# Performance work log

Measured on AMD Instinct MI355X. Metric: run time of the kernel, lower is better.

Reference implementation:

```python
import jax, jax.numpy as jnp
import numpy as np

N = 60000      # num_nodes
R = 70         # num_relations
B = 30         # num_bases
E = 1920000    # num_edges (avg degree 32)
STD = 0.1


def setup_inputs() -> dict:
    key = jax.random.key(0)
    ks = jax.random.split(key, 14)
    p = lambda k, shape: (jax.random.normal(k, shape, jnp.float32) * STD)
    inp = {}
    inp['edge_index'] = jax.random.randint(ks[0], (2, E), 0, N, dtype=jnp.int32)
    inp['edge_type'] = jax.random.randint(ks[1], (E,), 0, R, dtype=jnp.int32)
    # layer 1: in=N (identity features), out=32
    inp['att1'] = p(ks[2], (R, B))
    inp['basis1'] = p(ks[3], (B, N, 32))
    inp['root1'] = p(ks[4], (N, 32))
    inp['bias1'] = jnp.zeros((32,), jnp.float32)
    # layer 2: in=32, out=8
    inp['att2'] = p(ks[5], (R, B))
    inp['basis2'] = p(ks[6], (B, 32, 8))
    inp['root2'] = p(ks[7], (32, 8))
    inp['bias2'] = jnp.zeros((8,), jnp.float32)
    # layer 3: in=8, out=1
    inp['att3'] = p(ks[8], (R, B))
    inp['basis3'] = p(ks[9], (B, 8, 1))
    inp['root3'] = p(ks[10], (8, 1))
    inp['bias3'] = jnp.zeros((1,), jnp.float32)
    return inp


def _scatter_mean(msg, dst, num_nodes):
    s = jax.ops.segment_sum(msg, dst, num_segments=num_nodes)          # [N, O]
    cnt = jax.ops.segment_sum(jnp.ones((msg.shape[0], 1), msg.dtype), dst,
                              num_segments=num_nodes)                   # [N, 1]
    return s / jnp.maximum(cnt, 1.0)


def _rgcn(x, edge_index, edge_type, att, basis, root, bias, num_nodes):
    # basis decomposition: weight[r] = sum_b att[r,b] * basis[b]
    weight = jnp.einsum('rb,bio->rio', att, basis)  # [R, in, out]
    src, dst = edge_index[0], edge_index[1]
    if x is None:
        # identity input features -> message is a row of the relation weight
        msg = weight[edge_type, src]                # [E, out]
        self_term = root                            # x @ root with x = I
    else:
        # compute per-relation transforms once, then gather per edge
        h = jnp.einsum('ni,rio->rno', x, weight)    # [R, N, out]
        msg = h[edge_type, src]                     # [E, out]
        self_term = x @ root                        # [N, out]
    aggr = _scatter_mean(msg, dst, num_nodes)       # mean aggregation (old PyG RGCNConv)
    return aggr + self_term + bias


def reference(edge_index, edge_type, att1, basis1, root1, bias1,
              att2, basis2, root2, bias2, att3, basis3, root3, bias3):
    x = jax.nn.relu(_rgcn(None, edge_index, edge_type, att1, basis1, root1, bias1, N))
    x = jax.nn.relu(_rgcn(x, edge_index, edge_type, att2, basis2, root2, bias2, N))
    x = _rgcn(x, edge_index, edge_type, att3, basis3, root3, bias3, N)
    return x  # [N, 1]
```

## Files before the change

### kernel.cpp

```cpp
#include <hip/hip_runtime.h>
#include <hip/hip_bf16.h>
#include <hip/hip_fp16.h>

#define NNODES 60000
#define NREL   70
#define NB     30
#define NEDGE  1920000
#define NBLK   235
#define W2P    328

typedef _Float16 half2v __attribute__((ext_vector_type(2)));

static __device__ __forceinline__ float fdot2f(unsigned a, unsigned b, float c) {
    return __builtin_amdgcn_fdot2(__builtin_bit_cast(half2v, a),
                                  __builtin_bit_cast(half2v, b), c, false);
}
static __device__ __forceinline__ unsigned pack2h(float lo, float hi) {
    __half2 h = __floats2half2_rn(lo, hi);
    return *reinterpret_cast<unsigned*>(&h);
}


__global__ void hist2_kernel8(const int* __restrict__ src, const int* __restrict__ dst,
                              int* __restrict__ cntS, int* __restrict__ cntD,
                              int* __restrict__ ranks) {
    int g = blockIdx.x * blockDim.x + threadIdx.x;
    int e0 = g * 8;
    if (e0 >= NEDGE) return;
    int4 s0 = *reinterpret_cast<const int4*>(src + e0);
    int4 s1 = *reinterpret_cast<const int4*>(src + e0 + 4);
    int4 d0 = *reinterpret_cast<const int4*>(dst + e0);
    int4 d1 = *reinterpret_cast<const int4*>(dst + e0 + 4);
    int rS0 = atomicAdd(&cntS[s0.x], 1);
    int rS1 = atomicAdd(&cntS[s0.y], 1);
    int rS2 = atomicAdd(&cntS[s0.z], 1);
    int rS3 = atomicAdd(&cntS[s0.w], 1);
    int rS4 = atomicAdd(&cntS[s1.x], 1);
    int rS5 = atomicAdd(&cntS[s1.y], 1);
    int rS6 = atomicAdd(&cntS[s1.z], 1);
    int rS7 = atomicAdd(&cntS[s1.w], 1);
    int rD0 = atomicAdd(&cntD[d0.x], 1);
    int rD1 = atomicAdd(&cntD[d0.y], 1);
    int rD2 = atomicAdd(&cntD[d0.z], 1);
    int rD3 = atomicAdd(&cntD[d0.w], 1);
    int rD4 = atomicAdd(&cntD[d1.x], 1);
    int rD5 = atomicAdd(&cntD[d1.y], 1);
    int rD6 = atomicAdd(&cntD[d1.z], 1);
    int rD7 = atomicAdd(&cntD[d1.w], 1);
    int4 o0, o1;
    o0.x = (rD0 << 16) | rS0; o0.y = (rD1 << 16) | rS1;
    o0.z = (rD2 << 16) | rS2; o0.w = (rD3 << 16) | rS3;
    o1.x = (rD4 << 16) | rS4; o1.y = (rD5 << 16) | rS5;
    o1.z = (rD6 << 16) | rS6; o1.w = (rD7 << 16) | rS7;
    *reinterpret_cast<int4*>(ranks + e0)     = o0;
    *reinterpret_cast<int4*>(ranks + e0 + 4) = o1;
}

__global__ void scanA2_kernel(const int* __restrict__ cntS, const int* __restrict__ cntD,
                              int* __restrict__ bsum) {
    __shared__ int lds[256];
    int half = (blockIdx.x >= NBLK) ? 1 : 0;
    int blk  = blockIdx.x - half * NBLK;
    const int* cnt = half ? cntD : cntS;
    int i = blk * 256 + threadIdx.x;
    int v = (i < NNODES) ? cnt[i] : 0;
    lds[threadIdx.x] = v;
    __syncthreads();
    for (int d = 128; d > 0; d >>= 1) {
        if (threadIdx.x < d) lds[threadIdx.x] += lds[threadIdx.x + d];
        __syncthreads();
    }
    if (threadIdx.x == 0) bsum[half * 256 + blk] = lds[0];
}

__global__ void scanB2_kernel(const int* __restrict__ bsum, int* __restrict__ boff) {
    __shared__ int lds[256];
    for (int half = 0; half < 2; ++half) {
        int v = (threadIdx.x < NBLK) ? bsum[half * 256 + threadIdx.x] : 0;
        lds[threadIdx.x] = v;
        __syncthreads();
        for (int d = 1; d < 256; d <<= 1) {
            int t = (threadIdx.x >= d) ? lds[threadIdx.x - d] : 0;
            __syncthreads();
            lds[threadIdx.x] += t;
            __syncthreads();
        }
        boff[half * 256 + threadIdx.x] = lds[threadIdx.x] - v;
        __syncthreads();
    }
}

__global__ void scanC2_kernel(const int* __restrict__ cntS, const int* __restrict__ cntD,
                              const int* __restrict__ boff,
                              int* __restrict__ offsS, int* __restrict__ offsD) {
    __shared__ int lds[256];
    int half = (blockIdx.x >= NBLK) ? 1 : 0;
    int blk  = blockIdx.x - half * NBLK;
    const int* cnt = half ? cntD : cntS;
    int* offs = half ? offsD : offsS;
    int i = blk * 256 + threadIdx.x;
    int v = (i < NNODES) ? cnt[i] : 0;
    lds[threadIdx.x] = v;
    __syncthreads();
    for (int d = 1; d < 256; d <<= 1) {
        int t = (threadIdx.x >= d) ? lds[threadIdx.x - d] : 0;
        __syncthreads();
        lds[threadIdx.x] += t;
        __syncthreads();
    }
    if (i < NNODES) offs[i] = boff[half * 256 + blk] + lds[threadIdx.x] - v;
}

__global__ void fill2_stream_kernel8(const int* __restrict__ src, const int* __restrict__ dst,
                                     const int* __restrict__ et, const int* __restrict__ ranks,
                                     const int* __restrict__ offsS, const int* __restrict__ offsD,
                                     int2* __restrict__ ebufSD) {
    int g = blockIdx.x * blockDim.x + threadIdx.x;
    int e0 = g * 8;
    if (e0 >= NEDGE) return;
    int4 s0 = *reinterpret_cast<const int4*>(src + e0);
    int4 s1 = *reinterpret_cast<const int4*>(src + e0 + 4);
    int4 d0 = *reinterpret_cast<const int4*>(dst + e0);
    int4 d1 = *reinterpret_cast<const int4*>(dst + e0 + 4);
    int4 t0 = *reinterpret_cast<const int4*>(et + e0);
    int4 t1 = *reinterpret_cast<const int4*>(et + e0 + 4);
    int4 r0 = *reinterpret_cast<const int4*>(ranks + e0);
    int4 r1 = *reinterpret_cast<const int4*>(ranks + e0 + 4);
    int s[8] = {s0.x, s0.y, s0.z, s0.w, s1.x, s1.y, s1.z, s1.w};
    int d[8] = {d0.x, d0.y, d0.z, d0.w, d1.x, d1.y, d1.z, d1.w};
    int t[8] = {t0.x, t0.y, t0.z, t0.w, t1.x, t1.y, t1.z, t1.w};
    int r[8] = {r0.x, r0.y, r0.z, r0.w, r1.x, r1.y, r1.z, r1.w};
    int oS[8], oD[8];
    #pragma unroll
    for (int i = 0; i < 8; ++i) oS[i] = offsS[s[i]];
    #pragma unroll
    for (int i = 0; i < 8; ++i) oD[i] = offsD[d[i]];
    #pragma unroll
    for (int i = 0; i < 8; ++i) {
        int spos = oS[i] + (r[i] & 0xFFFF);
        int slot = oD[i] + (r[i] >> 16);
        ebufSD[spos] = make_int2((t[i] << 25) | slot, (t[i] << 16) | d[i]);
    }
}

__global__ void fill2_atomic_kernel(const int* __restrict__ src, const int* __restrict__ dst,
                                    const int* __restrict__ et, const int* __restrict__ ranks,
                                    const int* __restrict__ offsS, const int* __restrict__ offsD,
                                    int* __restrict__ ebufS, int* __restrict__ ebufD) {
    int e = blockIdx.x * blockDim.x + threadIdx.x;
    if (e < NEDGE) {
        int s = src[e], d = dst[e], t = et[e];
        int r = ranks[e];
        ebufD[offsD[d] + (r >> 16)]   = (t << 16) | s;
        ebufS[offsS[s] + (r & 0xFFFF)] = (t << 16) | d;
    }
}


__global__ void wexpand2_kernel(const float* __restrict__ att, const float* __restrict__ basis,
                                float* __restrict__ w2t) {
    int idx = blockIdx.x * blockDim.x + threadIdx.x;
    if (idx >= NREL * 256) return;
    int r = idx >> 8, t = idx & 255, o = t >> 5, i = t & 31;
    float s = 0.f;
    #pragma unroll
    for (int b = 0; b < NB; ++b) s += att[r * NB + b] * basis[b * 256 + i * 8 + o];
    w2t[r * 256 + o * 32 + i] = s;
}

__global__ void wexpand2h_kernel(const float* __restrict__ att, const float* __restrict__ basis,
                                 unsigned short* __restrict__ w2h) {
    int idx = blockIdx.x * blockDim.x + threadIdx.x;
    if (idx >= NREL * W2P) return;
    int r = idx / W2P, t = idx - r * W2P;
    int o = t / 40, i = t - o * 40;
    float s = 0.f;
    if (o < 8 && i < 32) {
        #pragma unroll
        for (int b = 0; b < NB; ++b) s += att[r * NB + b] * basis[b * 256 + i * 8 + o];
    }
    w2h[idx] = __half_as_ushort(__float2half_rn(s));
}

__global__ void wexpand3_kernel(const float* __restrict__ att, const float* __restrict__ basis,
                                float* __restrict__ w3) {
    int idx = blockIdx.x * blockDim.x + threadIdx.x;
    if (idx >= NREL * 8) return;
    int r = idx >> 3, i = idx & 7;
    float s = 0.f;
    #pragma unroll
    for (int b = 0; b < NB; ++b) s += att[r * NB + b] * basis[b * 8 + i];
    w3[idx] = s;
}


__global__ void layer1_scatter_stream_kernel(const int2* __restrict__ ebufSD,
                                             const int* __restrict__ offsS,
                                             const int* __restrict__ cntS,
                                             const float* __restrict__ att1,
                                             const float* __restrict__ basis1,
                                             unsigned short* __restrict__ msgh) {
    __shared__ unsigned att_lds[NREL * 16];
    for (int i = threadIdx.x; i < NREL * 16; i += 256) {
        int r = i >> 4, j = i & 15;
        float lo = (2 * j     < NB) ? att1[r * NB + 2 * j]     : 0.f;
        float hi = (2 * j + 1 < NB) ? att1[r * NB + 2 * j + 1] : 0.f;
        att_lds[i] = pack2h(lo, hi);
    }
    __syncthreads();
    int wave = threadIdx.x >> 6, lane = threadIdx.x & 63;
    int s = blockIdx.x * 4 + wave;
    int o = lane & 31, half = lane >> 5;
    int off = offsS[s], c = cntS[s];
    if (c == 0) return;
    float Bf[NB];
    const float* bp = basis1 + (size_t)s * 32 + o;
    #pragma unroll
    for (int b = 0; b < NB; ++b) Bf[b] = bp[(size_t)b * (NNODES * 32)];
    unsigned B2[16];
    #pragma unroll
    for (int q = 0; q < 15; ++q) B2[q] = pack2h(Bf[2 * q], Bf[2 * q + 1]);
    B2[15] = 0u;
    for (int k = half; k < c; k += 2) {
        unsigned p = (unsigned)ebufSD[off + k].x;
        int slot = p & 0x01FFFFFF;
        int et   = p >> 25;
        const uint4* ar = (const uint4*)(att_lds + et * 16);
        float m0 = 0.f, m1 = 0.f, m2 = 0.f, m3 = 0.f;
        #pragma unroll
        for (int q = 0; q < 4; ++q) {
            uint4 w = ar[q];
            m0 = fdot2f(w.x, B2[q * 4 + 0], m0);
            m1 = fdot2f(w.y, B2[q * 4 + 1], m1);
            m2 = fdot2f(w.z, B2[q * 4 + 2], m2);
            m3 = fdot2f(w.w, B2[q * 4 + 3], m3);
        }
        float m = (m0 + m1) + (m2 + m3);
        float mo = __shfl_xor(m, 1);
        if ((o & 1) == 0) {
            __half2 h;
            h.x = __float2half_rn(m);
            h.y = __float2half_rn(mo);
            *reinterpret_cast<__half2*>(msgh + (size_t)slot * 32 + o) = h;
        }
    }
}

__global__ void layer1_reduce_kernel(const unsigned short* __restrict__ msgh,
                                     const int* __restrict__ offsD, const int* __restrict__ cntD,
                                     const float* __restrict__ root1,
                                     const float* __restrict__ bias1,
                                     float* __restrict__ x1) {
    int wave = threadIdx.x >> 6, lane = threadIdx.x & 63;
    int n = blockIdx.x * 4 + wave;
    int o4 = (lane & 7) * 4, grp = lane >> 3;
    int off = offsD[n], c = cntD[n];
    float a0 = 0.f, a1 = 0.f, a2 = 0.f, a3 = 0.f;
    for (int k = grp; k < c; k += 8) {
        uint2 u = *reinterpret_cast<const uint2*>(msgh + (size_t)(off + k) * 32 + o4);
        __half2 h0 = *reinterpret_cast<__half2*>(&u.x);
        __half2 h1 = *reinterpret_cast<__half2*>(&u.y);
        float2 f0 = __half22float2(h0), f1 = __half22float2(h1);
        a0 += f0.x; a1 += f0.y; a2 += f1.x; a3 += f1.y;
    }
    a0 += __shfl_xor(a0, 8);  a1 += __shfl_xor(a1, 8);  a2 += __shfl_xor(a2, 8);  a3 += __shfl_xor(a3, 8);
    a0 += __shfl_xor(a0, 16); a1 += __shfl_xor(a1, 16); a2 += __shfl_xor(a2, 16); a3 += __shfl_xor(a3, 16);
    a0 += __shfl_xor(a0, 32); a1 += __shfl_xor(a1, 32); a2 += __shfl_xor(a2, 32); a3 += __shfl_xor(a3, 32);
    if (grp == 0) {
        float inv = 1.0f / fmaxf((float)c, 1.0f);
        size_t base = (size_t)n * 32 + o4;
        float4 r = *reinterpret_cast<const float4*>(root1 + base);
        float4 v;
        v.x = fmaxf(a0 * inv + r.x + bias1[o4],     0.f);
        v.y = fmaxf(a1 * inv + r.y + bias1[o4 + 1], 0.f);
        v.z = fmaxf(a2 * inv + r.z + bias1[o4 + 2], 0.f);
        v.w = fmaxf(a3 * inv + r.w + bias1[o4 + 3], 0.f);
        *reinterpret_cast<float4*>(x1 + base) = v;
    }
}


__global__ void layer1_scatter_kernel(const int* __restrict__ ebufS, const int* __restrict__ offsS,
                                      const int* __restrict__ cntS, const float* __restrict__ att1,
                                      const float* __restrict__ basis1, float* __restrict__ x1acc) {
    int wave = threadIdx.x >> 6, lane = threadIdx.x & 63;
    int s = blockIdx.x * 4 + wave;
    int o = lane & 31, half = lane >> 5;
    int off = offsS[s], c = cntS[s];
    if (c == 0) return;
    float B[NB];
    const float* bp = basis1 + (size_t)s * 32 + o;
    #pragma unroll
    for (int b = 0; b < NB; ++b) B[b] = bp[(size_t)b * (NNODES * 32)];
    for (int k = half; k < c; k += 2) {
        int p  = ebufS[off + k];
        int d  = p & 0xFFFF, et = p >> 16;
        float attv = (o < NB) ? att1[et * NB + o] : 0.f;
        float m = 0.f;
        #pragma unroll
        for (int b = 0; b < NB; ++b) {
            float a = __shfl(attv, (lane & 32) + b);
            m = fmaf(a, B[b], m);
        }
        atomicAdd(&x1acc[(size_t)d * 32 + o], m);
    }
}

__global__ void layer1_finalize_kernel(const int* __restrict__ cntD,
                                       const float* __restrict__ root1,
                                       const float* __restrict__ bias1,
                                       float* __restrict__ x1) {
    int i = blockIdx.x * 256 + threadIdx.x;
    if (i >= NNODES * 32) return;
    int n = i >> 5, o = i & 31;
    float c = (float)cntD[n];
    float v = x1[i] / fmaxf(c, 1.0f) + root1[i] + bias1[o];
    x1[i] = fmaxf(v, 0.0f);
}


__global__ void layer2_src_atomic_kernel(const int2* __restrict__ ebufSD,
                                         const int* __restrict__ offsS, const int* __restrict__ cntS,
                                         const float* __restrict__ x1,
                                         const unsigned short* __restrict__ w2h,
                                         float* __restrict__ x2acc) {
    __shared__ unsigned short w2l[NREL * W2P];
    for (int i = threadIdx.x; i < NREL * W2P; i += 1024) w2l[i] = w2h[i];
    __syncthreads();
    int wave = threadIdx.x >> 6, lane = threadIdx.x & 63;
    int s = blockIdx.x * 16 + wave;
    int o = lane & 7, grp = lane >> 3;
    int off = offsS[s], c = cntS[s];
    if (c == 0) return;
    float2 xf[16];
    const float2* xp2 = (const float2*)(x1 + (size_t)s * 32);
    #pragma unroll
    for (int i = 0; i < 16; ++i) xf[i] = xp2[i];
    for (int k0 = 0; k0 < c; k0 += 8) {
        int kk = k0 + grp;
        if (kk < c) {
            int p = ebufSD[off + kk].y;
            int d = p & 0xFFFF, et = p >> 16;
            const unsigned short* wp = w2l + et * W2P + o * 40;
            float a0 = 0.f, a1 = 0.f, a2 = 0.f, a3 = 0.f;
            #pragma unroll
            for (int q = 0; q < 4; ++q) {
                uint4 wv = *reinterpret_cast<const uint4*>(wp + q * 8);
                __half2 h; float2 f;
                h = *reinterpret_cast<const __half2*>(&wv.x); f = __half22float2(h);
                a0 = fmaf(xf[q * 4 + 0].x, f.x, a0); a0 = fmaf(xf[q * 4 + 0].y, f.y, a0);
                h = *reinterpret_cast<const __half2*>(&wv.y); f = __half22float2(h);
                a1 = fmaf(xf[q * 4 + 1].x, f.x, a1); a1 = fmaf(xf[q * 4 + 1].y, f.y, a1);
                h = *reinterpret_cast<const __half2*>(&wv.z); f = __half22float2(h);
                a2 = fmaf(xf[q * 4 + 2].x, f.x, a2); a2 = fmaf(xf[q * 4 + 2].y, f.y, a2);
                h = *reinterpret_cast<const __half2*>(&wv.w); f = __half22float2(h);
                a3 = fmaf(xf[q * 4 + 3].x, f.x, a3); a3 = fmaf(xf[q * 4 + 3].y, f.y, a3);
            }
            float acc = (a0 + a1) + (a2 + a3);
            atomicAdd(&x2acc[(size_t)d * 8 + o], acc);
        }
    }
}

__global__ void layer2_finalize_kernel(const int* __restrict__ cntD,
                                       const float* __restrict__ x1,
                                       const float* __restrict__ root2,
                                       const float* __restrict__ bias2,
                                       float* __restrict__ x2) {
    int t = blockIdx.x * 256 + threadIdx.x;
    if (t >= NNODES * 8) return;
    int n = t >> 3, o = t & 7;
    float self = 0.f;
    const float* xn = x1 + (size_t)n * 32;
    #pragma unroll
    for (int i = 0; i < 32; ++i) self = fmaf(xn[i], root2[i * 8 + o], self);
    float c = (float)cntD[n];
    float v = x2[t] / fmaxf(c, 1.0f) + self + bias2[o];
    x2[t] = fmaxf(v, 0.0f);
}


__global__ void layer3_src_atomic_kernel(const int2* __restrict__ ebufSD,
                                         const int* __restrict__ offsS, const int* __restrict__ cntS,
                                         const float* __restrict__ x2, const float* __restrict__ w3,
                                         float* __restrict__ outacc) {
    __shared__ float w3l[NREL * 8];
    for (int i = threadIdx.x; i < NREL * 8; i += 256) w3l[i] = w3[i];
    __syncthreads();
    int wave = threadIdx.x >> 6, lane = threadIdx.x & 63;
    int s = blockIdx.x * 4 + wave;
    int off = offsS[s], c = cntS[s];
    if (c == 0) return;
    const float4* xp = (const float4*)(x2 + (size_t)s * 8);
    float4 a0 = xp[0], a1 = xp[1];
    for (int k = lane; k < c; k += 64) {
        int p = ebufSD[off + k].y;
        int d = p & 0xFFFF, et = p >> 16;
        const float4* wp = (const float4*)(w3l + et * 8);
        float4 b0 = wp[0], b1 = wp[1];
        float m = a0.x * b0.x + a0.y * b0.y + a0.z * b0.z + a0.w * b0.w
                + a1.x * b1.x + a1.y * b1.y + a1.z * b1.z + a1.w * b1.w;
        atomicAdd(&outacc[d], m);
    }
}

__global__ void layer3_finalize_kernel(const int* __restrict__ cntD,
                                       const float* __restrict__ x2,
                                       const float* __restrict__ root3,
                                       const float* __restrict__ bias3,
                                       float* __restrict__ out) {
    int n = blockIdx.x * 256 + threadIdx.x;
    if (n >= NNODES) return;
    float self = 0.f;
    const float* xn = x2 + (size_t)n * 8;
    #pragma unroll
    for (int i = 0; i < 8; ++i) self = fmaf(xn[i], root3[i], self);
    float c = (float)cntD[n];
    out[n] = out[n] / fmaxf(c, 1.0f) + self + bias3[0];
}


__global__ void layer2_kernel(const int* __restrict__ ebufD, const int* __restrict__ offsD,
                              const int* __restrict__ cntD,
                              const float* __restrict__ x1, const float* __restrict__ w2t,
                              const float* __restrict__ root2, const float* __restrict__ bias2,
                              float* __restrict__ x2) {
    int wave = threadIdx.x >> 6, lane = threadIdx.x & 63;
    int n = blockIdx.x * 4 + wave;
    int o = lane & 7, slot = lane >> 3;
    int off = offsD[n], c = cntD[n];
    float acc = 0.f;
    for (int k0 = 0; k0 < c; k0 += 8) {
        int kk = k0 + slot;
        if (kk < c) {
            int packed = ebufD[off + kk];
            int src = packed & 0xFFFF, et = packed >> 16;
            const float4* xp = (const float4*)(x1 + (size_t)src * 32);
            const float4* wp = (const float4*)(w2t + et * 256 + o * 32);
            #pragma unroll
            for (int i = 0; i < 8; ++i) {
                float4 xv = xp[i], wv = wp[i];
                acc += xv.x * wv.x + xv.y * wv.y + xv.z * wv.z + xv.w * wv.w;
            }
        }
    }
    #pragma unroll
    for (int d = 8; d < 64; d <<= 1) acc += __shfl_xor(acc, d);
    if (lane < 8) {
        float self = 0.f;
        const float* xn = x1 + (size_t)n * 32;
        #pragma unroll
        for (int i = 0; i < 32; ++i) self += xn[i] * root2[i * 8 + o];
        float v = acc / fmaxf((float)c, 1.0f) + self + bias2[o];
        x2[(size_t)n * 8 + o] = fmaxf(v, 0.0f);
    }
}

__global__ void layer3_kernel(const int* __restrict__ ebufD, const int* __restrict__ offsD,
                              const int* __restrict__ cntD,
                              const float* __restrict__ x2, const float* __restrict__ w3,
                              const float* __restrict__ root3, const float* __restrict__ bias3,
                              float* __restrict__ out) {
    int wave = threadIdx.x >> 6, lane = threadIdx.x & 63;
    int n = blockIdx.x * 4 + wave;
    int off = offsD[n], c = cntD[n];
    float acc = 0.f;
    for (int k = lane; k < c; k += 64) {
        int packed = ebufD[off + k];
        int src = packed & 0xFFFF, et = packed >> 16;
        const float4* xp = (const float4*)(x2 + src * 8);
        const float4* wp = (const float4*)(w3 + et * 8);
        float4 a0 = xp[0], a1 = xp[1], b0 = wp[0], b1 = wp[1];
        acc += a0.x * b0.x + a0.y * b0.y + a0.z * b0.z + a0.w * b0.w
             + a1.x * b1.x + a1.y * b1.y + a1.z * b1.z + a1.w * b1.w;
    }
    #pragma unroll
    for (int d = 1; d < 64; d <<= 1) acc += __shfl_xor(acc, d);
    if (lane == 0) {
        float self = 0.f;
        const float* xn = x2 + (size_t)n * 8;
        #pragma unroll
        for (int i = 0; i < 8; ++i) self += xn[i] * root3[i];
        out[n] = acc / fmaxf((float)c, 1.0f) + self + bias3[0];
    }
}


extern "C" void kernel_launch(void* const* d_in, const int* in_sizes, int n_in,
                              void* d_out, int out_size, void* d_ws, size_t ws_size,
                              hipStream_t stream) {
    const int*   edge_index = (const int*)  d_in[0];
    const int*   edge_type  = (const int*)  d_in[1];
    const float* att1   = (const float*) d_in[2];
    const float* basis1 = (const float*) d_in[3];
    const float* root1  = (const float*) d_in[4];
    const float* bias1  = (const float*) d_in[5];
    const float* att2   = (const float*) d_in[6];
    const float* basis2 = (const float*) d_in[7];
    const float* root2  = (const float*) d_in[8];
    const float* bias2  = (const float*) d_in[9];
    const float* att3   = (const float*) d_in[10];
    const float* basis3 = (const float*) d_in[11];
    const float* root3  = (const float*) d_in[12];
    const float* bias3  = (const float*) d_in[13];
    float* out = (float*)d_out;

    const int* srcArr = edge_index;
    const int* dstArr = edge_index + NEDGE;

    char* ws = (char*)d_ws;
    int*   cntS   = (int*)(ws + 0);
    int*   cntD   = (int*)(ws + 240128);
    int*   offsS  = (int*)(ws + 480256);
    int*   offsD  = (int*)(ws + 720384);
    int*   bsum   = (int*)(ws + 960512);
    int*   boff   = (int*)(ws + 962560);
    int*   ebufS  = (int*)(ws + 1442816);
    int*   ebufD  = (int*)(ws + 9122816);
    int2*  ebufSD = (int2*)(ws + 1442816);
    float* w2t    = (float*)(ws + 16802816);
    float* w3     = (float*)(ws + 16874496);
    unsigned short* w2h = (unsigned short*)(ws + 16876800);
    float* x1     = (float*)(ws + 16923648);
    int*   ranks  = (int*)(ws + 16923648);
    float* x2     = (float*)(ws + 24603648);
    unsigned short* msgh = (unsigned short*)(ws + 26523648);
    const bool use_stream = ws_size >= 149403648ULL;

    hipMemsetAsync(ws, 0, 480128, stream);
    hipMemsetAsync((void*)x2, 0, 1920000, stream);
    hipMemsetAsync(d_out, 0, NNODES * 4, stream);

    hist2_kernel8<<<(NEDGE / 8 + 255) / 256, 256, 0, stream>>>(srcArr, dstArr, cntS, cntD, ranks);
    scanA2_kernel<<<2 * NBLK, 256, 0, stream>>>(cntS, cntD, bsum);
    scanB2_kernel<<<1, 256, 0, stream>>>(bsum, boff);
    scanC2_kernel<<<2 * NBLK, 256, 0, stream>>>(cntS, cntD, boff, offsS, offsD);
    if (use_stream) {
        fill2_stream_kernel8<<<(NEDGE / 8 + 255) / 256, 256, 0, stream>>>(srcArr, dstArr, edge_type,
                                                                          ranks, offsS, offsD, ebufSD);
    } else {
        fill2_atomic_kernel<<<NEDGE / 256, 256, 0, stream>>>(srcArr, dstArr, edge_type, ranks,
                                                             offsS, offsD, ebufS, ebufD);
    }

    wexpand2h_kernel<<<(NREL * W2P + 255) / 256, 256, 0, stream>>>(att2, basis2, w2h);
    wexpand3_kernel<<<(NREL * 8 + 255) / 256, 256, 0, stream>>>(att3, basis3, w3);
    if (!use_stream) {
        wexpand2_kernel<<<(NREL * 256 + 255) / 256, 256, 0, stream>>>(att2, basis2, w2t);
    }

    if (use_stream) {
        layer1_scatter_stream_kernel<<<NNODES / 4, 256, 0, stream>>>(ebufSD, offsS, cntS,
                                                                     att1, basis1, msgh);
        layer1_reduce_kernel<<<NNODES / 4, 256, 0, stream>>>(msgh, offsD, cntD, root1, bias1, x1);
    } else {
        hipMemsetAsync((void*)x1, 0, 7680000, stream);
        layer1_scatter_kernel<<<NNODES / 4, 256, 0, stream>>>(ebufS, offsS, cntS, att1, basis1, x1);
        layer1_finalize_kernel<<<(NNODES * 32) / 256, 256, 0, stream>>>(cntD, root1, bias1, x1);
    }

    if (use_stream) {
        layer2_src_atomic_kernel<<<NNODES / 16, 1024, 0, stream>>>(ebufSD, offsS, cntS, x1, w2h, x2);
        layer2_finalize_kernel<<<(NNODES * 8 + 255) / 256, 256, 0, stream>>>(cntD, x1, root2, bias2, x2);
        layer3_src_atomic_kernel<<<NNODES / 4, 256, 0, stream>>>(ebufSD, offsS, cntS, x2, w3, out);
        layer3_finalize_kernel<<<(NNODES + 255) / 256, 256, 0, stream>>>(cntD, x2, root3, bias3, out);
    } else {
        layer2_kernel<<<NNODES / 4, 256, 0, stream>>>(ebufD, offsD, cntD, x1, w2t, root2, bias2, x2);
        layer3_kernel<<<NNODES / 4, 256, 0, stream>>>(ebufD, offsD, cntD, x2, w3, root3, bias3, out);
    }
}
```

Before: 617.3 us.

## Split interleaved edge buffer into src-sorted list and dst-to-src position map

Replaces the packed int2 source-sorted edge buffer with two int arrays: a src-sorted (type,dst) array and a dst-sorted array of source positions. Layer 1 scatter now writes messages contiguously in source order instead of scattering to dst slots, and the reduce kernel gathers through the position indirection. This halves the edge record read in layers 2/3 and makes message writes coalesced, in exchange for an extra index load and scattered message reads in the reduce step.

```diff
diff --git a/kernel.cpp b/kernel.cpp
--- a/kernel.cpp
+++ b/kernel.cpp
@@ -114,7 +114,7 @@
 __global__ void fill2_stream_kernel8(const int* __restrict__ src, const int* __restrict__ dst,
                                      const int* __restrict__ et, const int* __restrict__ ranks,
                                      const int* __restrict__ offsS, const int* __restrict__ offsD,
-                                     int2* __restrict__ ebufSD) {
+                                     int* __restrict__ ebufA, int* __restrict__ ebufB) {
     int g = blockIdx.x * blockDim.x + threadIdx.x;
     int e0 = g * 8;
     if (e0 >= NEDGE) return;
@@ -139,7 +139,8 @@
     for (int i = 0; i < 8; ++i) {
         int spos = oS[i] + (r[i] & 0xFFFF);
         int slot = oD[i] + (r[i] >> 16);
-        ebufSD[spos] = make_int2((t[i] << 25) | slot, (t[i] << 16) | d[i]);
+        ebufA[spos] = (t[i] << 16) | d[i];
+        ebufB[slot] = spos;
     }
 }
 
@@ -194,7 +195,7 @@
 }
 
 
-__global__ void layer1_scatter_stream_kernel(const int2* __restrict__ ebufSD,
+__global__ void layer1_scatter_stream_kernel(const int* __restrict__ ebufA,
                                              const int* __restrict__ offsS,
                                              const int* __restrict__ cntS,
                                              const float* __restrict__ att1,
@@ -222,9 +223,7 @@
     for (int q = 0; q < 15; ++q) B2[q] = pack2h(Bf[2 * q], Bf[2 * q + 1]);
     B2[15] = 0u;
     for (int k = half; k < c; k += 2) {
-        unsigned p = (unsigned)ebufSD[off + k].x;
-        int slot = p & 0x01FFFFFF;
-        int et   = p >> 25;
+        int et = ebufA[off + k] >> 16;
         const uint4* ar = (const uint4*)(att_lds + et * 16);
         float m0 = 0.f, m1 = 0.f, m2 = 0.f, m3 = 0.f;
         #pragma unroll
@@ -241,12 +240,13 @@
             __half2 h;
             h.x = __float2half_rn(m);
             h.y = __float2half_rn(mo);
-            *reinterpret_cast<__half2*>(msgh + (size_t)slot * 32 + o) = h;
+            *reinterpret_cast<__half2*>(msgh + (size_t)(off + k) * 32 + o) = h;
         }
     }
 }
 
 __global__ void layer1_reduce_kernel(const unsigned short* __restrict__ msgh,
+                                     const int* __restrict__ ebufB,
                                      const int* __restrict__ offsD, const int* __restrict__ cntD,
                                      const float* __restrict__ root1,
                                      const float* __restrict__ bias1,
@@ -257,7 +257,8 @@
     int off = offsD[n], c = cntD[n];
     float a0 = 0.f, a1 = 0.f, a2 = 0.f, a3 = 0.f;
     for (int k = grp; k < c; k += 8) {
-        uint2 u = *reinterpret_cast<const uint2*>(msgh + (size_t)(off + k) * 32 + o4);
+        int spos = ebufB[off + k];
+        uint2 u = *reinterpret_cast<const uint2*>(msgh + (size_t)spos * 32 + o4);
         __half2 h0 = *reinterpret_cast<__half2*>(&u.x);
         __half2 h1 = *reinterpret_cast<__half2*>(&u.y);
         float2 f0 = __half22float2(h0), f1 = __half22float2(h1);
@@ -319,7 +320,7 @@
 }
 
 
-__global__ void layer2_src_atomic_kernel(const int2* __restrict__ ebufSD,
+__global__ void layer2_src_atomic_kernel(const int* __restrict__ ebufA,
                                          const int* __restrict__ offsS, const int* __restrict__ cntS,
                                          const float* __restrict__ x1,
                                          const unsigned short* __restrict__ w2h,
@@ -339,7 +340,7 @@
     for (int k0 = 0; k0 < c; k0 += 8) {
         int kk = k0 + grp;
         if (kk < c) {
-            int p = ebufSD[off + kk].y;
+            int p = ebufA[off + kk];
             int d = p & 0xFFFF, et = p >> 16;
             const unsigned short* wp = w2l + et * W2P + o * 40;
             float a0 = 0.f, a1 = 0.f, a2 = 0.f, a3 = 0.f;
@@ -380,7 +381,7 @@
 }
 
 
-__global__ void layer3_src_atomic_kernel(const int2* __restrict__ ebufSD,
+__global__ void layer3_src_atomic_kernel(const int* __restrict__ ebufA,
                                          const int* __restrict__ offsS, const int* __restrict__ cntS,
                                          const float* __restrict__ x2, const float* __restrict__ w3,
                                          float* __restrict__ outacc) {
@@ -394,7 +395,7 @@
     const float4* xp = (const float4*)(x2 + (size_t)s * 8);
     float4 a0 = xp[0], a1 = xp[1];
     for (int k = lane; k < c; k += 64) {
-        int p = ebufSD[off + k].y;
+        int p = ebufA[off + k];
         int d = p & 0xFFFF, et = p >> 16;
         const float4* wp = (const float4*)(w3l + et * 8);
         float4 b0 = wp[0], b1 = wp[1];
@@ -515,9 +516,8 @@
     int*   offsD  = (int*)(ws + 720384);
     int*   bsum   = (int*)(ws + 960512);
     int*   boff   = (int*)(ws + 962560);
-    int*   ebufS  = (int*)(ws + 1442816);
-    int*   ebufD  = (int*)(ws + 9122816);
-    int2*  ebufSD = (int2*)(ws + 1442816);
+    int*   ebufA  = (int*)(ws + 1442816);
+    int*   ebufB  = (int*)(ws + 9122816);
     float* w2t    = (float*)(ws + 16802816);
     float* w3     = (float*)(ws + 16874496);
     unsigned short* w2h = (unsigned short*)(ws + 16876800);
@@ -537,10 +537,11 @@
     scanC2_kernel<<<2 * NBLK, 256, 0, stream>>>(cntS, cntD, boff, offsS, offsD);
     if (use_stream) {
         fill2_stream_kernel8<<<(NEDGE / 8 + 255) / 256, 256, 0, stream>>>(srcArr, dstArr, edge_type,
-                                                                          ranks, offsS, offsD, ebufSD);
+                                                                          ranks, offsS, offsD,
+                                                                          ebufA, ebufB);
     } else {
         fill2_atomic_kernel<<<NEDGE / 256, 256, 0, stream>>>(srcArr, dstArr, edge_type, ranks,
-                                                             offsS, offsD, ebufS, ebufD);
+                                                             offsS, offsD, ebufA, ebufB);
     }
 
     wexpand2h_kernel<<<(NREL * W2P + 255) / 256, 256, 0, stream>>>(att2, basis2, w2h);
@@ -550,22 +551,23 @@
     }
 
     if (use_stream) {
-        layer1_scatter_stream_kernel<<<NNODES / 4, 256, 0, stream>>>(ebufSD, offsS, cntS,
+        layer1_scatter_stream_kernel<<<NNODES / 4, 256, 0, stream>>>(ebufA, offsS, cntS,
                                                                      att1, basis1, msgh);
-        layer1_reduce_kernel<<<NNODES / 4, 256, 0, stream>>>(msgh, offsD, cntD, root1, bias1, x1);
+        layer1_reduce_kernel<<<NNODES / 4, 256, 0, stream>>>(msgh, ebufB, offsD, cntD,
+                                                             root1, bias1, x1);
     } else {
         hipMemsetAsync((void*)x1, 0, 7680000, stream);
-        layer1_scatter_kernel<<<NNODES / 4, 256, 0, stream>>>(ebufS, offsS, cntS, att1, basis1, x1);
+        layer1_scatter_kernel<<<NNODES / 4, 256, 0, stream>>>(ebufA, offsS, cntS, att1, basis1, x1);
         layer1_finalize_kernel<<<(NNODES * 32) / 256, 256, 0, stream>>>(cntD, root1, bias1, x1);
     }
 
     if (use_stream) {
-        layer2_src_atomic_kernel<<<NNODES / 16, 1024, 0, stream>>>(ebufSD, offsS, cntS, x1, w2h, x2);
+        layer2_src_atomic_kernel<<<NNODES / 16, 1024, 0, stream>>>(ebufA, offsS, cntS, x1, w2h, x2);
         layer2_finalize_kernel<<<(NNODES * 8 + 255) / 256, 256, 0, stream>>>(cntD, x1, root2, bias2, x2);
-        layer3_src_atomic_kernel<<<NNODES / 4, 256, 0, stream>>>(ebufSD, offsS, cntS, x2, w3, out);
+        layer3_src_atomic_kernel<<<NNODES / 4, 256, 0, stream>>>(ebufA, offsS, cntS, x2, w3, out);
         layer3_finalize_kernel<<<(NNODES + 255) / 256, 256, 0, stream>>>(cntD, x2, root3, bias3, out);
     } else {
-        layer2_kernel<<<NNODES / 4, 256, 0, stream>>>(ebufD, offsD, cntD, x1, w2t, root2, bias2, x2);
-        layer3_kernel<<<NNODES / 4, 256, 0, stream>>>(ebufD, offsD, cntD, x2, w3, root3, bias3, out);
-    }
-}
+        layer2_kernel<<<NNODES / 4, 256, 0, stream>>>(ebufB, offsD, cntD, x1, w2t, root2, bias2, x2);
+        layer3_kernel<<<NNODES / 4, 256, 0, stream>>>(ebufB, offsD, cntD, x2, w3, root3, bias3, out);
+    }
+}
```

Result: slower. 639.3 us (+3.6%).
